# Performance work log

Hardware: AMD Instinct MI355X
Metric: run time of the kernel (lower is better)

Reference implementation:

```python
import jax, jax.numpy as jnp
import numpy as np

TOP_K = 8


def setup_inputs() -> dict:
    key = jax.random.key(0)
    k1, k2, k3 = jax.random.split(key, 3)
    tokens, hidden, experts = 32768, 2048, 64
    hidden_states = jax.random.normal(k1, (tokens, hidden), dtype=jnp.float32)
    weight = jax.random.normal(k2, (experts, hidden), dtype=jnp.float32) * 0.02
    bias = jax.random.normal(k3, (experts,), dtype=jnp.float32) * 0.02
    return {"hidden_states": hidden_states, "weight": weight, "bias": bias}


def reference(hidden_states, weight, bias):
    # router logits: [tokens, experts]
    logits = jnp.einsum('th,eh->te', hidden_states, weight) + bias
    top_vals, top_idx = jax.lax.top_k(logits, TOP_K)            # [tokens, k]
    top_probs = jax.nn.softmax(top_vals, axis=-1)               # softmax over selected k
    rows = jnp.arange(logits.shape[0])[:, None]                  # [tokens, 1]
    scores = jnp.zeros_like(logits).at[rows, top_idx].set(top_probs)
    return scores, top_idx
```

## Files before the change

### kernel.cpp

```cpp
#include <hip/hip_runtime.h>
#include <math.h>

typedef _Float16 half8 __attribute__((ext_vector_type(8)));
typedef _Float16 half4 __attribute__((ext_vector_type(4)));
typedef float    f32x4 __attribute__((ext_vector_type(4)));

#define TOKENS  32768
#define HIDDEN  2048
#define EXPERTS 64
#define TOPK    8
#define BKW     64
#define NWIN    (HIDDEN / BKW)
#define LDH     72

__global__ void wsplit(const float* __restrict__ W,
                       _Float16* __restrict__ whi, _Float16* __restrict__ wlo) {
    int i = blockIdx.x * 256 + threadIdx.x;
    float w = W[i];
    _Float16 h = (_Float16)w;
    whi[i] = h;
    wlo[i] = (_Float16)(w - (float)h);
}

__global__ __launch_bounds__(256, 1)
void router_mfma(const float* __restrict__ A,
                 const _Float16* __restrict__ Wh,
                 const _Float16* __restrict__ Wl,
                 const float* __restrict__ bias,
                 float* __restrict__ out) {
    __shared__ __align__(16) _Float16 hsm[4 * 64 * LDH];
    _Float16* Ahs = hsm;
    _Float16* Als = hsm + 64 * LDH;
    _Float16* Whs = hsm + 2 * 64 * LDH;
    _Float16* Wls = hsm + 3 * 64 * LDH;

    const int tid = threadIdx.x;
    const int w   = tid >> 6;
    const int l   = tid & 63;
    const int g   = blockIdx.x;

    const int s_tok = tid >> 4;
    const int s_c   = tid & 15;
    const int we = tid >> 2;
    const int wc = tid & 3;

    const float* Abase = A + (size_t)g * 64 * HIDDEN;

    f32x4 acc[4];
    #pragma unroll
    for (int n = 0; n < 4; ++n) acc[n] = (f32x4){0.f, 0.f, 0.f, 0.f};

    float4 ar0, ar1, ar2, ar3;
    half8 wrh0, wrh1, wrl0, wrl1;

    #define LOADA(win) do {                                                  \
        const float* p_ = Abase + (size_t)(win) * BKW + s_c * 4;             \
        ar0 = *(const float4*)(p_ + (size_t)(s_tok     ) * HIDDEN);          \
        ar1 = *(const float4*)(p_ + (size_t)(s_tok + 16) * HIDDEN);          \
        ar2 = *(const float4*)(p_ + (size_t)(s_tok + 32) * HIDDEN);          \
        ar3 = *(const float4*)(p_ + (size_t)(s_tok + 48) * HIDDEN);          \
    } while (0)

    #define LOADW(win) do {                                                  \
        const _Float16* ph_ = Wh + (size_t)we * HIDDEN + (win) * BKW;        \
        const _Float16* pl_ = Wl + (size_t)we * HIDDEN + (win) * BKW;        \
        wrh0 = *(const half8*)(ph_ + wc * 8);                                \
        wrh1 = *(const half8*)(ph_ + wc * 8 + 32);                           \
        wrl0 = *(const half8*)(pl_ + wc * 8);                                \
        wrl1 = *(const half8*)(pl_ + wc * 8 + 32);                           \
    } while (0)

    #define STAGE1(v, trow) do {                                             \
        _Float16 h0_ = (_Float16)(v).x, h1_ = (_Float16)(v).y;               \
        _Float16 h2_ = (_Float16)(v).z, h3_ = (_Float16)(v).w;               \
        half4 hh_ = {h0_, h1_, h2_, h3_};                                    \
        half4 ll_ = {(_Float16)((v).x - (float)h0_),                         \
                     (_Float16)((v).y - (float)h1_),                         \
                     (_Float16)((v).z - (float)h2_),                         \
                     (_Float16)((v).w - (float)h3_)};                        \
        *(half4*)(&Ahs[(trow) * LDH + s_c * 4]) = hh_;                       \
        *(half4*)(&Als[(trow) * LDH + s_c * 4]) = ll_;                       \
    } while (0)

    LOADA(0);
    LOADW(0);

    #pragma unroll 1
    for (int win = 0; win < NWIN; ++win) {
        __syncthreads();
        STAGE1(ar0, s_tok);
        STAGE1(ar1, s_tok + 16);
        STAGE1(ar2, s_tok + 32);
        STAGE1(ar3, s_tok + 48);
        *(half8*)(&Whs[we * LDH + wc * 8])      = wrh0;
        *(half8*)(&Whs[we * LDH + wc * 8 + 32]) = wrh1;
        *(half8*)(&Wls[we * LDH + wc * 8])      = wrl0;
        *(half8*)(&Wls[we * LDH + wc * 8 + 32]) = wrl1;
        __syncthreads();

        if (win + 1 < NWIN) {
            LOADA(win + 1);
            LOADW(win + 1);
        }

        #pragma unroll
        for (int ks = 0; ks < 2; ++ks) {
            const int ko = ks * 32 + (l >> 4) * 8;
            half8 ahi = *(const half8*)(&Ahs[(w * 16 + (l & 15)) * LDH + ko]);
            half8 alo = *(const half8*)(&Als[(w * 16 + (l & 15)) * LDH + ko]);
            #pragma unroll
            for (int n = 0; n < 4; ++n) {
                half8 bh = *(const half8*)(&Whs[(n * 16 + (l & 15)) * LDH + ko]);
                half8 bl = *(const half8*)(&Wls[(n * 16 + (l & 15)) * LDH + ko]);
                acc[n] = __builtin_amdgcn_mfma_f32_16x16x32_f16(ahi, bh, acc[n], 0, 0, 0);
                acc[n] = __builtin_amdgcn_mfma_f32_16x16x32_f16(ahi, bl, acc[n], 0, 0, 0);
                acc[n] = __builtin_amdgcn_mfma_f32_16x16x32_f16(alo, bh, acc[n], 0, 0, 0);
            }
        }
    }
    #undef LOADA
    #undef LOADW
    #undef STAGE1

    __syncthreads();
    float* lg = (float*)hsm;
    float* sc = (float*)hsm + 64 * 68;

    #pragma unroll
    for (int n = 0; n < 4; ++n) {
        float b = bias[n * 16 + (l & 15)];
        #pragma unroll
        for (int q = 0; q < 4; ++q) {
            int trow = w * 16 + (l >> 4) * 4 + q;
            lg[trow * 68 + n * 16 + (l & 15)] = acc[n][q] + b;
        }
    }
    for (int i = tid; i < 64 * 65; i += 256) sc[i] = 0.f;
    __syncthreads();

    if (tid < 64) {
        const int t = tid;
        float v[64];
        #pragma unroll
        for (int e = 0; e < 64; ++e) v[e] = lg[t * 68 + e];

        float tvals[TOPK]; int tix[TOPK]; float probs[TOPK];
        unsigned long long chosen = 0ull;
        #pragma unroll
        for (int j = 0; j < TOPK; ++j) {
            float best = -INFINITY; int bi = 0;
            #pragma unroll
            for (int e = 0; e < 64; ++e) {
                bool ok = ((chosen >> e) & 1ull) == 0ull;
                if (ok && v[e] > best) { best = v[e]; bi = e; }
            }
            chosen |= (1ull << bi);
            tvals[j] = best; tix[j] = bi;
        }
        float m = tvals[0];
        float ssum = 0.f;
        #pragma unroll
        for (int j = 0; j < TOPK; ++j) { probs[j] = __expf(tvals[j] - m); ssum += probs[j]; }
        float inv = 1.f / ssum;
        #pragma unroll
        for (int j = 0; j < TOPK; ++j) probs[j] *= inv;

        #pragma unroll
        for (int j = 0; j < TOPK; ++j) sc[t * 65 + tix[j]] = probs[j];

        float* oidx = out + (size_t)TOKENS * EXPERTS;
        const int token = g * 64 + t;
        #pragma unroll
        for (int j = 0; j < TOPK; ++j) oidx[(size_t)token * TOPK + j] = (float)tix[j];
    }
    __syncthreads();

    float* oscore = out + (size_t)g * 4096;
    #pragma unroll
    for (int p = 0; p < 4; ++p) {
        int fi  = tid + 256 * p;
        int tok = fi >> 4;
        int es  = (fi & 15) * 4;
        float4 vv;
        vv.x = sc[tok * 65 + es + 0];
        vv.y = sc[tok * 65 + es + 1];
        vv.z = sc[tok * 65 + es + 2];
        vv.w = sc[tok * 65 + es + 3];
        *(float4*)(oscore + (size_t)fi * 4) = vv;
    }
}

extern "C" void kernel_launch(void* const* d_in, const int* in_sizes, int n_in,
                              void* d_out, int out_size, void* d_ws, size_t ws_size,
                              hipStream_t stream) {
    const float* A    = (const float*)d_in[0];
    const float* W    = (const float*)d_in[1];
    const float* bias = (const float*)d_in[2];
    float* out = (float*)d_out;

    _Float16* whi = (_Float16*)d_ws;
    _Float16* wlo = whi + EXPERTS * HIDDEN;

    wsplit<<<512, 256, 0, stream>>>(W, whi, wlo);
    router_mfma<<<TOKENS / 64, 256, 0, stream>>>(A, whi, wlo, bias, out);
}
```

Measured before the change: 64.84 us.

## Split router GEMM across eight waves per block with expert halves

Doubles the block to 512 threads so eight waves share each 64-token tile. Each wave now computes 16 tokens by 32 experts instead of 16 by 64, and the global-to-LDS staging is spread over twice as many threads, halving per-thread load and convert work. The goal is more latency hiding and more MFMA issue parallelism per CU on this memory-bound, 512-block grid. In exchange each block carries more threads through the barrier-heavy loop, and the top-k epilogue still runs on a single wave.

```diff
diff --git a/kernel.cpp b/kernel.cpp
--- a/kernel.cpp
+++ b/kernel.cpp
@@ -22,12 +22,12 @@
     wlo[i] = (_Float16)(w - (float)h);
 }
 
-__global__ __launch_bounds__(256, 1)
-void router_mfma(const float* __restrict__ A,
-                 const _Float16* __restrict__ Wh,
-                 const _Float16* __restrict__ Wl,
-                 const float* __restrict__ bias,
-                 float* __restrict__ out) {
+__global__ __launch_bounds__(512, 1)
+void router_mfma8(const float* __restrict__ A,
+                  const _Float16* __restrict__ Wh,
+                  const _Float16* __restrict__ Wl,
+                  const float* __restrict__ bias,
+                  float* __restrict__ out) {
     __shared__ __align__(16) _Float16 hsm[4 * 64 * LDH];
     _Float16* Ahs = hsm;
     _Float16* Als = hsm + 64 * LDH;
@@ -35,42 +35,37 @@
     _Float16* Wls = hsm + 3 * 64 * LDH;
 
     const int tid = threadIdx.x;
-    const int w   = tid >> 6;
+    const int wv  = tid >> 6;
     const int l   = tid & 63;
     const int g   = blockIdx.x;
+    const int ts  = wv & 3;
+    const int eh  = wv >> 2;
 
-    const int s_tok = tid >> 4;
-    const int s_c   = tid & 15;
-    const int we = tid >> 2;
-    const int wc = tid & 3;
+    const int ar = tid >> 3;
+    const int ac = tid & 7;
+    const int wr = tid >> 3;
+    const int wc = tid & 7;
 
-    const float* Abase = A + (size_t)g * 64 * HIDDEN;
+    const float*    Abase  = A  + ((size_t)g * 64 + ar) * HIDDEN;
+    const _Float16* WhBase = Wh + (size_t)wr * HIDDEN;
+    const _Float16* WlBase = Wl + (size_t)wr * HIDDEN;
 
-    f32x4 acc[4];
-    #pragma unroll
-    for (int n = 0; n < 4; ++n) acc[n] = (f32x4){0.f, 0.f, 0.f, 0.f};
+    f32x4 acc[2];
+    acc[0] = (f32x4){0.f, 0.f, 0.f, 0.f};
+    acc[1] = (f32x4){0.f, 0.f, 0.f, 0.f};
 
-    float4 ar0, ar1, ar2, ar3;
-    half8 wrh0, wrh1, wrl0, wrl1;
+    float4 a0r, a1r;
+    half8 whr, wlr;
 
     #define LOADA(win) do {                                                  \
-        const float* p_ = Abase + (size_t)(win) * BKW + s_c * 4;             \
-        ar0 = *(const float4*)(p_ + (size_t)(s_tok     ) * HIDDEN);          \
-        ar1 = *(const float4*)(p_ + (size_t)(s_tok + 16) * HIDDEN);          \
-        ar2 = *(const float4*)(p_ + (size_t)(s_tok + 32) * HIDDEN);          \
-        ar3 = *(const float4*)(p_ + (size_t)(s_tok + 48) * HIDDEN);          \
+        a0r = *(const float4*)(Abase + (win) * BKW + ac * 4);                \
+        a1r = *(const float4*)(Abase + (win) * BKW + (ac + 8) * 4);          \
     } while (0)
-
     #define LOADW(win) do {                                                  \
-        const _Float16* ph_ = Wh + (size_t)we * HIDDEN + (win) * BKW;        \
-        const _Float16* pl_ = Wl + (size_t)we * HIDDEN + (win) * BKW;        \
-        wrh0 = *(const half8*)(ph_ + wc * 8);                                \
-        wrh1 = *(const half8*)(ph_ + wc * 8 + 32);                           \
-        wrl0 = *(const half8*)(pl_ + wc * 8);                                \
-        wrl1 = *(const half8*)(pl_ + wc * 8 + 32);                           \
+        whr = *(const half8*)(WhBase + (win) * BKW + wc * 8);                \
+        wlr = *(const half8*)(WlBase + (win) * BKW + wc * 8);                \
     } while (0)
-
-    #define STAGE1(v, trow) do {                                             \
+    #define CVT1(v, col) do {                                                \
         _Float16 h0_ = (_Float16)(v).x, h1_ = (_Float16)(v).y;               \
         _Float16 h2_ = (_Float16)(v).z, h3_ = (_Float16)(v).w;               \
         half4 hh_ = {h0_, h1_, h2_, h3_};                                    \
@@ -78,8 +73,8 @@
                      (_Float16)((v).y - (float)h1_),                         \
                      (_Float16)((v).z - (float)h2_),                         \
                      (_Float16)((v).w - (float)h3_)};                        \
-        *(half4*)(&Ahs[(trow) * LDH + s_c * 4]) = hh_;                       \
-        *(half4*)(&Als[(trow) * LDH + s_c * 4]) = ll_;                       \
+        *(half4*)(&Ahs[ar * LDH + (col) * 4]) = hh_;                         \
+        *(half4*)(&Als[ar * LDH + (col) * 4]) = ll_;                         \
     } while (0)
 
     LOADA(0);
@@ -88,14 +83,10 @@
     #pragma unroll 1
     for (int win = 0; win < NWIN; ++win) {
         __syncthreads();
-        STAGE1(ar0, s_tok);
-        STAGE1(ar1, s_tok + 16);
-        STAGE1(ar2, s_tok + 32);
-        STAGE1(ar3, s_tok + 48);
-        *(half8*)(&Whs[we * LDH + wc * 8])      = wrh0;
-        *(half8*)(&Whs[we * LDH + wc * 8 + 32]) = wrh1;
-        *(half8*)(&Wls[we * LDH + wc * 8])      = wrl0;
-        *(half8*)(&Wls[we * LDH + wc * 8 + 32]) = wrl1;
+        CVT1(a0r, ac);
+        CVT1(a1r, ac + 8);
+        *(half8*)(&Whs[wr * LDH + wc * 8]) = whr;
+        *(half8*)(&Wls[wr * LDH + wc * 8]) = wlr;
         __syncthreads();
 
         if (win + 1 < NWIN) {
@@ -106,12 +97,13 @@
         #pragma unroll
         for (int ks = 0; ks < 2; ++ks) {
             const int ko = ks * 32 + (l >> 4) * 8;
-            half8 ahi = *(const half8*)(&Ahs[(w * 16 + (l & 15)) * LDH + ko]);
-            half8 alo = *(const half8*)(&Als[(w * 16 + (l & 15)) * LDH + ko]);
+            half8 ahi = *(const half8*)(&Ahs[(ts * 16 + (l & 15)) * LDH + ko]);
+            half8 alo = *(const half8*)(&Als[(ts * 16 + (l & 15)) * LDH + ko]);
             #pragma unroll
-            for (int n = 0; n < 4; ++n) {
-                half8 bh = *(const half8*)(&Whs[(n * 16 + (l & 15)) * LDH + ko]);
-                half8 bl = *(const half8*)(&Wls[(n * 16 + (l & 15)) * LDH + ko]);
+            for (int n = 0; n < 2; ++n) {
+                const int brow = eh * 32 + n * 16 + (l & 15);
+                half8 bh = *(const half8*)(&Whs[brow * LDH + ko]);
+                half8 bl = *(const half8*)(&Wls[brow * LDH + ko]);
                 acc[n] = __builtin_amdgcn_mfma_f32_16x16x32_f16(ahi, bh, acc[n], 0, 0, 0);
                 acc[n] = __builtin_amdgcn_mfma_f32_16x16x32_f16(ahi, bl, acc[n], 0, 0, 0);
                 acc[n] = __builtin_amdgcn_mfma_f32_16x16x32_f16(alo, bh, acc[n], 0, 0, 0);
@@ -120,22 +112,23 @@
     }
     #undef LOADA
     #undef LOADW
-    #undef STAGE1
+    #undef CVT1
 
     __syncthreads();
     float* lg = (float*)hsm;
     float* sc = (float*)hsm + 64 * 68;
 
     #pragma unroll
-    for (int n = 0; n < 4; ++n) {
-        float b = bias[n * 16 + (l & 15)];
+    for (int n = 0; n < 2; ++n) {
+        const int ecol = eh * 32 + n * 16 + (l & 15);
+        float b = bias[ecol];
         #pragma unroll
         for (int q = 0; q < 4; ++q) {
-            int trow = w * 16 + (l >> 4) * 4 + q;
-            lg[trow * 68 + n * 16 + (l & 15)] = acc[n][q] + b;
+            int trow = ts * 16 + (l >> 4) * 4 + q;
+            lg[trow * 68 + ecol] = acc[n][q] + b;
         }
     }
-    for (int i = tid; i < 64 * 65; i += 256) sc[i] = 0.f;
+    for (int i = tid; i < 64 * 65; i += 512) sc[i] = 0.f;
     __syncthreads();
 
     if (tid < 64) {
@@ -177,8 +170,8 @@
 
     float* oscore = out + (size_t)g * 4096;
     #pragma unroll
-    for (int p = 0; p < 4; ++p) {
-        int fi  = tid + 256 * p;
+    for (int p = 0; p < 2; ++p) {
+        int fi  = tid + 512 * p;
         int tok = fi >> 4;
         int es  = (fi & 15) * 4;
         float4 vv;
@@ -202,5 +195,5 @@
     _Float16* wlo = whi + EXPERTS * HIDDEN;
 
     wsplit<<<512, 256, 0, stream>>>(W, whi, wlo);
-    router_mfma<<<TOKENS / 64, 256, 0, stream>>>(A, whi, wlo, bias, out);
+    router_mfma8<<<TOKENS / 64, 512, 0, stream>>>(A, whi, wlo, bias, out);
 }
```

After: 67.32 us. 3.8% more time.

## Double-buffer LDS tiles and prefetch two windows ahead in router GEMM

Applied to the files above, without the earlier changes.

Replaces the single LDS buffer with two ping-pong buffers and two register staging sets. Global loads run two windows ahead, and LDS stores for the next window overlap the MFMA compute on the current one, so each window needs one barrier instead of two. In exchange, LDS use doubles (about 72 KB) and register pressure rises from the second staging set, which could hurt occupancy or cause spills.

```diff
diff --git a/kernel.cpp b/kernel.cpp
--- a/kernel.cpp
+++ b/kernel.cpp
@@ -12,6 +12,7 @@
 #define BKW     64
 #define NWIN    (HIDDEN / BKW)
 #define LDH     72
+#define BUFH    (4 * 64 * LDH)
 
 __global__ void wsplit(const float* __restrict__ W,
                        _Float16* __restrict__ whi, _Float16* __restrict__ wlo) {
@@ -23,17 +24,12 @@
 }
 
 __global__ __launch_bounds__(256, 1)
-void router_mfma(const float* __restrict__ A,
-                 const _Float16* __restrict__ Wh,
-                 const _Float16* __restrict__ Wl,
-                 const float* __restrict__ bias,
-                 float* __restrict__ out) {
-    __shared__ __align__(16) _Float16 hsm[4 * 64 * LDH];
-    _Float16* Ahs = hsm;
-    _Float16* Als = hsm + 64 * LDH;
-    _Float16* Whs = hsm + 2 * 64 * LDH;
-    _Float16* Wls = hsm + 3 * 64 * LDH;
-
+void router_db(const float* __restrict__ A,
+               const _Float16* __restrict__ Wh,
+               const _Float16* __restrict__ Wl,
+               const float* __restrict__ bias,
+               float* __restrict__ out) {
+    __shared__ __align__(16) _Float16 hsm[2 * BUFH];
     const int tid = threadIdx.x;
     const int w   = tid >> 6;
     const int l   = tid & 63;
@@ -41,36 +37,33 @@
 
     const int s_tok = tid >> 4;
     const int s_c   = tid & 15;
-    const int we = tid >> 2;
-    const int wc = tid & 3;
-
-    const float* Abase = A + (size_t)g * 64 * HIDDEN;
+    const int we    = tid >> 2;
+    const int wc    = tid & 3;
+
+    const float*    Abase = A + (size_t)g * 64 * HIDDEN;
+    const _Float16* WhB   = Wh + (size_t)we * HIDDEN;
+    const _Float16* WlB   = Wl + (size_t)we * HIDDEN;
 
     f32x4 acc[4];
     #pragma unroll
     for (int n = 0; n < 4; ++n) acc[n] = (f32x4){0.f, 0.f, 0.f, 0.f};
 
-    float4 ar0, ar1, ar2, ar3;
-    half8 wrh0, wrh1, wrl0, wrl1;
-
-    #define LOADA(win) do {                                                  \
+    float4 aA0, aA1, aA2, aA3;  half8 wAh0, wAh1, wAl0, wAl1;
+    float4 aB0, aB1, aB2, aB3;  half8 wBh0, wBh1, wBl0, wBl1;
+
+    #define LOADS(S, win) do {                                               \
         const float* p_ = Abase + (size_t)(win) * BKW + s_c * 4;             \
-        ar0 = *(const float4*)(p_ + (size_t)(s_tok     ) * HIDDEN);          \
-        ar1 = *(const float4*)(p_ + (size_t)(s_tok + 16) * HIDDEN);          \
-        ar2 = *(const float4*)(p_ + (size_t)(s_tok + 32) * HIDDEN);          \
-        ar3 = *(const float4*)(p_ + (size_t)(s_tok + 48) * HIDDEN);          \
-    } while (0)
-
-    #define LOADW(win) do {                                                  \
-        const _Float16* ph_ = Wh + (size_t)we * HIDDEN + (win) * BKW;        \
-        const _Float16* pl_ = Wl + (size_t)we * HIDDEN + (win) * BKW;        \
-        wrh0 = *(const half8*)(ph_ + wc * 8);                                \
-        wrh1 = *(const half8*)(ph_ + wc * 8 + 32);                           \
-        wrl0 = *(const half8*)(pl_ + wc * 8);                                \
-        wrl1 = *(const half8*)(pl_ + wc * 8 + 32);                           \
-    } while (0)
-
-    #define STAGE1(v, trow) do {                                             \
+        a##S##0 = *(const float4*)(p_ + (size_t)(s_tok     ) * HIDDEN);      \
+        a##S##1 = *(const float4*)(p_ + (size_t)(s_tok + 16) * HIDDEN);      \
+        a##S##2 = *(const float4*)(p_ + (size_t)(s_tok + 32) * HIDDEN);      \
+        a##S##3 = *(const float4*)(p_ + (size_t)(s_tok + 48) * HIDDEN);      \
+        w##S##h0 = *(const half8*)(WhB + (win) * BKW + wc * 8);              \
+        w##S##h1 = *(const half8*)(WhB + (win) * BKW + wc * 8 + 32);         \
+        w##S##l0 = *(const half8*)(WlB + (win) * BKW + wc * 8);              \
+        w##S##l1 = *(const half8*)(WlB + (win) * BKW + wc * 8 + 32);         \
+    } while (0)
+
+    #define CVT1(B, v, trow) do {                                            \
         _Float16 h0_ = (_Float16)(v).x, h1_ = (_Float16)(v).y;               \
         _Float16 h2_ = (_Float16)(v).z, h3_ = (_Float16)(v).w;               \
         half4 hh_ = {h0_, h1_, h2_, h3_};                                    \
@@ -78,51 +71,60 @@
                      (_Float16)((v).y - (float)h1_),                         \
                      (_Float16)((v).z - (float)h2_),                         \
                      (_Float16)((v).w - (float)h3_)};                        \
-        *(half4*)(&Ahs[(trow) * LDH + s_c * 4]) = hh_;                       \
-        *(half4*)(&Als[(trow) * LDH + s_c * 4]) = ll_;                       \
-    } while (0)
-
-    LOADA(0);
-    LOADW(0);
+        *(half4*)(&hsm[(B) + (trow) * LDH + s_c * 4]) = hh_;                 \
+        *(half4*)(&hsm[(B) + 64 * LDH + (trow) * LDH + s_c * 4]) = ll_;      \
+    } while (0)
+
+    #define STORES(S, B) do {                                                \
+        CVT1(B, a##S##0, s_tok);                                             \
+        CVT1(B, a##S##1, s_tok + 16);                                        \
+        CVT1(B, a##S##2, s_tok + 32);                                        \
+        CVT1(B, a##S##3, s_tok + 48);                                        \
+        *(half8*)(&hsm[(B) + 2 * 64 * LDH + we * LDH + wc * 8])      = w##S##h0; \
+        *(half8*)(&hsm[(B) + 2 * 64 * LDH + we * LDH + wc * 8 + 32]) = w##S##h1; \
+        *(half8*)(&hsm[(B) + 3 * 64 * LDH + we * LDH + wc * 8])      = w##S##l0; \
+        *(half8*)(&hsm[(B) + 3 * 64 * LDH + we * LDH + wc * 8 + 32]) = w##S##l1; \
+    } while (0)
+
+    #define COMPUTE(B) do {                                                  \
+        _Pragma("unroll")                                                    \
+        for (int ks = 0; ks < 2; ++ks) {                                     \
+            const int ko = ks * 32 + (l >> 4) * 8;                           \
+            half8 ahi = *(const half8*)(&hsm[(B) + (w * 16 + (l & 15)) * LDH + ko]); \
+            half8 alo = *(const half8*)(&hsm[(B) + 64 * LDH + (w * 16 + (l & 15)) * LDH + ko]); \
+            _Pragma("unroll")                                                \
+            for (int n = 0; n < 4; ++n) {                                    \
+                half8 bh = *(const half8*)(&hsm[(B) + 2 * 64 * LDH + (n * 16 + (l & 15)) * LDH + ko]); \
+                half8 bl = *(const half8*)(&hsm[(B) + 3 * 64 * LDH + (n * 16 + (l & 15)) * LDH + ko]); \
+                acc[n] = __builtin_amdgcn_mfma_f32_16x16x32_f16(ahi, bh, acc[n], 0, 0, 0); \
+                acc[n] = __builtin_amdgcn_mfma_f32_16x16x32_f16(ahi, bl, acc[n], 0, 0, 0); \
+                acc[n] = __builtin_amdgcn_mfma_f32_16x16x32_f16(alo, bh, acc[n], 0, 0, 0); \
+            }                                                                \
+        }                                                                    \
+    } while (0)
+
+    LOADS(A, 0);
+    STORES(A, 0);
+    LOADS(A, 1);
+    __syncthreads();
 
     #pragma unroll 1
-    for (int win = 0; win < NWIN; ++win) {
+    for (int s = 0; s < NWIN; s += 2) {
+        if (s + 2 < NWIN) LOADS(B, s + 2);
+        COMPUTE(0);
+        if (s + 1 < NWIN) STORES(A, BUFH);
         __syncthreads();
-        STAGE1(ar0, s_tok);
-        STAGE1(ar1, s_tok + 16);
-        STAGE1(ar2, s_tok + 32);
-        STAGE1(ar3, s_tok + 48);
-        *(half8*)(&Whs[we * LDH + wc * 8])      = wrh0;
-        *(half8*)(&Whs[we * LDH + wc * 8 + 32]) = wrh1;
-        *(half8*)(&Wls[we * LDH + wc * 8])      = wrl0;
-        *(half8*)(&Wls[we * LDH + wc * 8 + 32]) = wrl1;
+
+        if (s + 3 < NWIN) LOADS(A, s + 3);
+        COMPUTE(BUFH);
+        if (s + 2 < NWIN) STORES(B, 0);
         __syncthreads();
-
-        if (win + 1 < NWIN) {
-            LOADA(win + 1);
-            LOADW(win + 1);
-        }
-
-        #pragma unroll
-        for (int ks = 0; ks < 2; ++ks) {
-            const int ko = ks * 32 + (l >> 4) * 8;
-            half8 ahi = *(const half8*)(&Ahs[(w * 16 + (l & 15)) * LDH + ko]);
-            half8 alo = *(const half8*)(&Als[(w * 16 + (l & 15)) * LDH + ko]);
-            #pragma unroll
-            for (int n = 0; n < 4; ++n) {
-                half8 bh = *(const half8*)(&Whs[(n * 16 + (l & 15)) * LDH + ko]);
-                half8 bl = *(const half8*)(&Wls[(n * 16 + (l & 15)) * LDH + ko]);
-                acc[n] = __builtin_amdgcn_mfma_f32_16x16x32_f16(ahi, bh, acc[n], 0, 0, 0);
-                acc[n] = __builtin_amdgcn_mfma_f32_16x16x32_f16(ahi, bl, acc[n], 0, 0, 0);
-                acc[n] = __builtin_amdgcn_mfma_f32_16x16x32_f16(alo, bh, acc[n], 0, 0, 0);
-            }
-        }
-    }
-    #undef LOADA
-    #undef LOADW
-    #undef STAGE1
-
-    __syncthreads();
+    }
+    #undef LOADS
+    #undef CVT1
+    #undef STORES
+    #undef COMPUTE
+
     float* lg = (float*)hsm;
     float* sc = (float*)hsm + 64 * 68;
 
@@ -202,5 +204,5 @@
     _Float16* wlo = whi + EXPERTS * HIDDEN;
 
     wsplit<<<512, 256, 0, stream>>>(W, whi, wlo);
-    router_mfma<<<TOKENS / 64, 256, 0, stream>>>(A, whi, wlo, bias, out);
+    router_db<<<TOKENS / 64, 256, 0, stream>>>(A, whi, wlo, bias, out);
 }
```

Result: slower. 69.98 us (+7.9%).

## Load A directly into MFMA register layout and double-buffer W in LDS

Applied to the files above, without the earlier changes.

Each lane now loads its own A fragment straight from global memory in the layout the MFMA operand needs, converting it to hi/lo fp16 in registers instead of staging A through LDS. A is prefetched two windows ahead, and W is double-buffered in LDS, which removes one barrier per window. This cuts LDS traffic and synchronisation in a kernel that is bound by streaming A. In exchange each lane issues more scattered 32-byte global loads and holds more registers.

```diff
diff --git a/kernel.cpp b/kernel.cpp
--- a/kernel.cpp
+++ b/kernel.cpp
@@ -2,7 +2,6 @@
 #include <math.h>
 
 typedef _Float16 half8 __attribute__((ext_vector_type(8)));
-typedef _Float16 half4 __attribute__((ext_vector_type(4)));
 typedef float    f32x4 __attribute__((ext_vector_type(4)));
 
 #define TOKENS  32768
@@ -12,6 +11,7 @@
 #define BKW     64
 #define NWIN    (HIDDEN / BKW)
 #define LDH     72
+#define WBUF    (2 * 64 * LDH)
 
 __global__ void wsplit(const float* __restrict__ W,
                        _Float16* __restrict__ whi, _Float16* __restrict__ wlo) {
@@ -23,106 +23,113 @@
 }
 
 __global__ __launch_bounds__(256, 1)
-void router_mfma(const float* __restrict__ A,
-                 const _Float16* __restrict__ Wh,
-                 const _Float16* __restrict__ Wl,
-                 const float* __restrict__ bias,
-                 float* __restrict__ out) {
-    __shared__ __align__(16) _Float16 hsm[4 * 64 * LDH];
-    _Float16* Ahs = hsm;
-    _Float16* Als = hsm + 64 * LDH;
-    _Float16* Whs = hsm + 2 * 64 * LDH;
-    _Float16* Wls = hsm + 3 * 64 * LDH;
-
+void router_hyb(const float* __restrict__ A,
+                const _Float16* __restrict__ Wh,
+                const _Float16* __restrict__ Wl,
+                const float* __restrict__ bias,
+                float* __restrict__ out) {
+    __shared__ __align__(16) _Float16 hsm[2 * WBUF];
     const int tid = threadIdx.x;
-    const int w   = tid >> 6;
+    const int wv  = tid >> 6;
     const int l   = tid & 63;
     const int g   = blockIdx.x;
 
-    const int s_tok = tid >> 4;
-    const int s_c   = tid & 15;
     const int we = tid >> 2;
     const int wc = tid & 3;
-
-    const float* Abase = A + (size_t)g * 64 * HIDDEN;
+    const _Float16* WhB = Wh + (size_t)we * HIDDEN;
+    const _Float16* WlB = Wl + (size_t)we * HIDDEN;
+
+    const float* pa = A + ((size_t)(g * 64 + wv * 16 + (l & 15))) * HIDDEN + (l >> 4) * 8;
+
+    const int ko0 = (l >> 4) * 8;
+    const int ko1 = 32 + ko0;
 
     f32x4 acc[4];
     #pragma unroll
     for (int n = 0; n < 4; ++n) acc[n] = (f32x4){0.f, 0.f, 0.f, 0.f};
 
-    float4 ar0, ar1, ar2, ar3;
-    half8 wrh0, wrh1, wrl0, wrl1;
-
-    #define LOADA(win) do {                                                  \
-        const float* p_ = Abase + (size_t)(win) * BKW + s_c * 4;             \
-        ar0 = *(const float4*)(p_ + (size_t)(s_tok     ) * HIDDEN);          \
-        ar1 = *(const float4*)(p_ + (size_t)(s_tok + 16) * HIDDEN);          \
-        ar2 = *(const float4*)(p_ + (size_t)(s_tok + 32) * HIDDEN);          \
-        ar3 = *(const float4*)(p_ + (size_t)(s_tok + 48) * HIDDEN);          \
+    float4 aA0, aA1, aA2, aA3;
+    float4 aB0, aB1, aB2, aB3;
+    half8 swh0, swh1, swl0, swl1;
+
+    #define LOADA(S, win) do {                                               \
+        const float* p_ = pa + (win) * BKW;                                  \
+        a##S##0 = *(const float4*)(p_);                                      \
+        a##S##1 = *(const float4*)(p_ + 4);                                  \
+        a##S##2 = *(const float4*)(p_ + 32);                                 \
+        a##S##3 = *(const float4*)(p_ + 36);                                 \
     } while (0)
 
     #define LOADW(win) do {                                                  \
-        const _Float16* ph_ = Wh + (size_t)we * HIDDEN + (win) * BKW;        \
-        const _Float16* pl_ = Wl + (size_t)we * HIDDEN + (win) * BKW;        \
-        wrh0 = *(const half8*)(ph_ + wc * 8);                                \
-        wrh1 = *(const half8*)(ph_ + wc * 8 + 32);                           \
-        wrl0 = *(const half8*)(pl_ + wc * 8);                                \
-        wrl1 = *(const half8*)(pl_ + wc * 8 + 32);                           \
-    } while (0)
-
-    #define STAGE1(v, trow) do {                                             \
-        _Float16 h0_ = (_Float16)(v).x, h1_ = (_Float16)(v).y;               \
-        _Float16 h2_ = (_Float16)(v).z, h3_ = (_Float16)(v).w;               \
-        half4 hh_ = {h0_, h1_, h2_, h3_};                                    \
-        half4 ll_ = {(_Float16)((v).x - (float)h0_),                         \
-                     (_Float16)((v).y - (float)h1_),                         \
-                     (_Float16)((v).z - (float)h2_),                         \
-                     (_Float16)((v).w - (float)h3_)};                        \
-        *(half4*)(&Ahs[(trow) * LDH + s_c * 4]) = hh_;                       \
-        *(half4*)(&Als[(trow) * LDH + s_c * 4]) = ll_;                       \
-    } while (0)
-
-    LOADA(0);
+        swh0 = *(const half8*)(WhB + (win) * BKW + wc * 8);                  \
+        swh1 = *(const half8*)(WhB + (win) * BKW + wc * 8 + 32);             \
+        swl0 = *(const half8*)(WlB + (win) * BKW + wc * 8);                  \
+        swl1 = *(const half8*)(WlB + (win) * BKW + wc * 8 + 32);             \
+    } while (0)
+
+    #define STOREW(B) do {                                                   \
+        *(half8*)(&hsm[(B) + we * LDH + wc * 8])                = swh0;      \
+        *(half8*)(&hsm[(B) + we * LDH + wc * 8 + 32])           = swh1;      \
+        *(half8*)(&hsm[(B) + 64 * LDH + we * LDH + wc * 8])      = swl0;     \
+        *(half8*)(&hsm[(B) + 64 * LDH + we * LDH + wc * 8 + 32]) = swl1;     \
+    } while (0)
+
+    #define CVT8(HI, LO, V0, V1) do {                                        \
+        float f_[8] = {(V0).x, (V0).y, (V0).z, (V0).w,                       \
+                       (V1).x, (V1).y, (V1).z, (V1).w};                      \
+        _Pragma("unroll")                                                    \
+        for (int j_ = 0; j_ < 8; ++j_) {                                     \
+            _Float16 h_ = (_Float16)f_[j_];                                  \
+            (HI)[j_] = h_;                                                   \
+            (LO)[j_] = (_Float16)(f_[j_] - (float)h_);                       \
+        }                                                                    \
+    } while (0)
+
+    #define MFMA_STEP(B, AH, AL, KO) do {                                    \
+        _Pragma("unroll")                                                    \
+        for (int n = 0; n < 4; ++n) {                                        \
+            half8 bh = *(const half8*)(&hsm[(B) + (n * 16 + (l & 15)) * LDH + (KO)]); \
+            half8 bl = *(const half8*)(&hsm[(B) + 64 * LDH + (n * 16 + (l & 15)) * LDH + (KO)]); \
+            acc[n] = __builtin_amdgcn_mfma_f32_16x16x32_f16(AH, bh, acc[n], 0, 0, 0); \
+            acc[n] = __builtin_amdgcn_mfma_f32_16x16x32_f16(AH, bl, acc[n], 0, 0, 0); \
+            acc[n] = __builtin_amdgcn_mfma_f32_16x16x32_f16(AL, bh, acc[n], 0, 0, 0); \
+        }                                                                    \
+    } while (0)
+
+    #define PHASE(B, S, win) do {                                            \
+        half8 ahi0, alo0, ahi1, alo1;                                        \
+        CVT8(ahi0, alo0, a##S##0, a##S##1);                                  \
+        CVT8(ahi1, alo1, a##S##2, a##S##3);                                  \
+        if ((win) + 2 < NWIN) LOADA(S, (win) + 2);   \
+        MFMA_STEP(B, ahi0, alo0, ko0);                                       \
+        MFMA_STEP(B, ahi1, alo1, ko1);                                       \
+    } while (0)
+
+    LOADA(A, 0);
+    LOADA(B, 1);
     LOADW(0);
+    STOREW(0);
+    __syncthreads();
 
     #pragma unroll 1
-    for (int win = 0; win < NWIN; ++win) {
+    for (int s = 0; s < NWIN; s += 2) {
+        if (s + 1 < NWIN) LOADW(s + 1);
+        PHASE(0, A, s);
+        if (s + 1 < NWIN) STOREW(WBUF);
         __syncthreads();
-        STAGE1(ar0, s_tok);
-        STAGE1(ar1, s_tok + 16);
-        STAGE1(ar2, s_tok + 32);
-        STAGE1(ar3, s_tok + 48);
-        *(half8*)(&Whs[we * LDH + wc * 8])      = wrh0;
-        *(half8*)(&Whs[we * LDH + wc * 8 + 32]) = wrh1;
-        *(half8*)(&Wls[we * LDH + wc * 8])      = wrl0;
-        *(half8*)(&Wls[we * LDH + wc * 8 + 32]) = wrl1;
+
+        if (s + 2 < NWIN) LOADW(s + 2);
+        PHASE(WBUF, B, s + 1);
+        if (s + 2 < NWIN) STOREW(0);
         __syncthreads();
-
-        if (win + 1 < NWIN) {
-            LOADA(win + 1);
-            LOADW(win + 1);
-        }
-
-        #pragma unroll
-        for (int ks = 0; ks < 2; ++ks) {
-            const int ko = ks * 32 + (l >> 4) * 8;
-            half8 ahi = *(const half8*)(&Ahs[(w * 16 + (l & 15)) * LDH + ko]);
-            half8 alo = *(const half8*)(&Als[(w * 16 + (l & 15)) * LDH + ko]);
-            #pragma unroll
-            for (int n = 0; n < 4; ++n) {
-                half8 bh = *(const half8*)(&Whs[(n * 16 + (l & 15)) * LDH + ko]);
-                half8 bl = *(const half8*)(&Wls[(n * 16 + (l & 15)) * LDH + ko]);
-                acc[n] = __builtin_amdgcn_mfma_f32_16x16x32_f16(ahi, bh, acc[n], 0, 0, 0);
-                acc[n] = __builtin_amdgcn_mfma_f32_16x16x32_f16(ahi, bl, acc[n], 0, 0, 0);
-                acc[n] = __builtin_amdgcn_mfma_f32_16x16x32_f16(alo, bh, acc[n], 0, 0, 0);
-            }
-        }
     }
     #undef LOADA
     #undef LOADW
-    #undef STAGE1
-
-    __syncthreads();
+    #undef STOREW
+    #undef CVT8
+    #undef MFMA_STEP
+    #undef PHASE
+
     float* lg = (float*)hsm;
     float* sc = (float*)hsm + 64 * 68;
 
@@ -131,7 +138,7 @@
         float b = bias[n * 16 + (l & 15)];
         #pragma unroll
         for (int q = 0; q < 4; ++q) {
-            int trow = w * 16 + (l >> 4) * 4 + q;
+            int trow = wv * 16 + (l >> 4) * 4 + q;
             lg[trow * 68 + n * 16 + (l & 15)] = acc[n][q] + b;
         }
     }
@@ -202,5 +209,5 @@
     _Float16* wlo = whi + EXPERTS * HIDDEN;
 
     wsplit<<<512, 256, 0, stream>>>(W, whi, wlo);
-    router_mfma<<<TOKENS / 64, 256, 0, stream>>>(A, whi, wlo, bias, out);
+    router_hyb<<<TOKENS / 64, 256, 0, stream>>>(A, whi, wlo, bias, out);
 }
```

New measurement: 69.21 us. 1.07x slower.
